# Kernel optimization log

Measured on AMD Instinct MI355X. Metric: run time of the kernel, lower is better.

## Reference

```python
import jax, jax.numpy as jnp
import numpy as np

B, N, GN, GS = 16, 100000, 4096, 64  # batch, points, num_groups, group_size


def setup_inputs() -> dict:
    key = jax.random.key(0)
    k1, k2, k3 = jax.random.split(key, 3)
    x_proto = jax.random.normal(k1, (B, N, 3), dtype=jnp.float32)
    template = jax.random.normal(k2, (N, 3), dtype=jnp.float32)
    groups = jax.random.randint(k3, (GN, GS), 0, N, dtype=jnp.int32)
    return {"x_proto": x_proto, "template": template, "groups": groups}


def reference(x_proto, template, groups):
    # x_proto: [B, N, 3], template: [N, 3], groups: [GN, GS] int indices
    b, n, _ = x_proto.shape
    Yg = template[groups]                      # [GN, GS, 3] gathered template
    Xg = x_proto[:, groups]                    # [B, GN, GS, 3] gathered current points

    # Kabsch: align template group Y to current X (R @ Y + t ~ X)
    muY = Yg.mean(axis=1)                      # [GN, 3]
    muX = Xg.mean(axis=2)                      # [B, GN, 3]
    Yc = Yg - muY[:, None, :]
    Xc = Xg - muX[:, :, None, :]
    H = jnp.einsum('gni,bgnj->bgij', Yc, Xc)   # [B, GN, 3, 3] covariance
    U, S, Vh = jnp.linalg.svd(H)
    V = jnp.swapaxes(Vh, -2, -1)
    R0 = V @ jnp.swapaxes(U, -2, -1)
    det = jnp.linalg.det(R0)                   # [B, GN]
    # flip last column of V where det < 0 to get a proper rotation
    s = jnp.where(det < 0, -1.0, 1.0).astype(x_proto.dtype)
    col_scale = jnp.stack([jnp.ones_like(s), jnp.ones_like(s), s], axis=-1)  # [B, GN, 3]
    R = (V * col_scale[..., None, :]) @ jnp.swapaxes(U, -2, -1)              # [B, GN, 3, 3]
    t = muX - jnp.einsum('bgij,gj->bgi', R, muY)                             # [B, GN, 3]

    # project template group through (R, t)
    Xg_proj = jnp.einsum('bgij,gnj->bgni', R, Yg) + t[:, :, None, :]         # [B, GN, GS, 3]

    # scatter-add with overlap counting, then average
    flat_idx = groups.reshape(-1)              # [GN*GS]
    out = jnp.zeros_like(x_proto).at[:, flat_idx].add(Xg_proj.reshape(b, -1, 3))
    counts = jnp.zeros((n,), dtype=x_proto.dtype).at[flat_idx].add(1.0)
    counts = jnp.maximum(counts, 1.0)
    return out / counts[None, :, None]
```

## Files before the change

### kernel.cpp

```cpp
#include <hip/hip_runtime.h>
#include <math.h>

static constexpr int BB = 16;
static constexpr int NN = 100000;
static constexpr int GN = 4096;
static constexpr int GS = 64;
static constexpr int NP = BB * GN;
static constexpr int SLOT = 32;

__device__ __forceinline__ float wsum64(float v) {
#pragma unroll
  for (int off = 32; off > 0; off >>= 1) v += __shfl_xor(v, off, 64);
  return v;
}

__global__ __launch_bounds__(256) void k_xpad(
    const float4* __restrict__ x, float4* __restrict__ x4,
    int4* __restrict__ cnt4) {
  int t = blockIdx.x * 256 + threadIdx.x;
  if (t < NN / 4) cnt4[t] = make_int4(0, 0, 0, 0);
  if (t >= BB * NN / 4) return;
  float4 a = x[t * 3 + 0], b = x[t * 3 + 1], c = x[t * 3 + 2];
  x4[t * 4 + 0] = make_float4(a.x, a.y, a.z, 0.f);
  x4[t * 4 + 1] = make_float4(a.w, b.x, b.y, 0.f);
  x4[t * 4 + 2] = make_float4(b.z, b.w, c.x, 0.f);
  x4[t * 4 + 3] = make_float4(c.y, c.z, c.w, 0.f);
}

__global__ __launch_bounds__(256) void k_tpl(
    const float* __restrict__ tpl, const int* __restrict__ groups,
    float* __restrict__ Yg, float* __restrict__ GmY,
    int* __restrict__ cnt, int* __restrict__ ent) {
  int g    = blockIdx.x * 4 + (threadIdx.x >> 6);
  int lane = threadIdx.x & 63;
  int idx = groups[g * GS + lane];
  int pos = atomicAdd(&cnt[idx], 1);
  if (pos < SLOT) ent[idx * SLOT + pos] = g;
  float y0 = tpl[idx * 3 + 0], y1 = tpl[idx * 3 + 1], y2 = tpl[idx * 3 + 2];
  float* o = Yg + ((size_t)g * GS + lane) * 3;
  o[0] = y0; o[1] = y1; o[2] = y2;
  float sy0 = wsum64(y0), sy1 = wsum64(y1), sy2 = wsum64(y2);
  if (lane == 0) {
    const float inv = 1.0f / 64.0f;
    *(float4*)(GmY + (size_t)g * 4) =
        make_float4(sy0 * inv, sy1 * inv, sy2 * inv, 0.0f);
  }
}

__global__ __launch_bounds__(256) void k_stats(
    const float4* __restrict__ x4, const float* __restrict__ Yg,
    const float* __restrict__ GmY, const int* __restrict__ groups,
    float* __restrict__ Ht) {
  int bid  = (blockIdx.x & 7) * 512 + (blockIdx.x >> 3);
  int wid4 = bid * 4 + (threadIdx.x >> 6);
  int lane = threadIdx.x & 63;
  int s    = lane >> 4;
  int l4   = lane & 15;
  int p = wid4 * 4 + s;
  int b = p >> 12;
  int g = p & (GN - 1);

  int4 iv = *(const int4*)(groups + (size_t)g * GS + l4 * 4);
  const float4* yv = (const float4*)(Yg + ((size_t)g * GS + l4 * 4) * 3);
  float4 ya = yv[0], yb = yv[1], yc = yv[2];

  const float4* xb4 = x4 + (size_t)b * NN;
  float sx0 = 0.f, sx1 = 0.f, sx2 = 0.f;
  float h00 = 0.f, h01 = 0.f, h02 = 0.f;
  float h10 = 0.f, h11 = 0.f, h12 = 0.f;
  float h20 = 0.f, h21 = 0.f, h22 = 0.f;

#define ACC(Y0, Y1, Y2, IDX)                                   \
  {                                                            \
    float4 xv = xb4[IDX];                                      \
    sx0 += xv.x; sx1 += xv.y; sx2 += xv.z;                     \
    h00 += (Y0) * xv.x; h01 += (Y0) * xv.y; h02 += (Y0) * xv.z;\
    h10 += (Y1) * xv.x; h11 += (Y1) * xv.y; h12 += (Y1) * xv.z;\
    h20 += (Y2) * xv.x; h21 += (Y2) * xv.y; h22 += (Y2) * xv.z;\
  }
  ACC(ya.x, ya.y, ya.z, iv.x);
  ACC(ya.w, yb.x, yb.y, iv.y);
  ACC(yb.z, yb.w, yc.x, iv.z);
  ACC(yc.y, yc.z, yc.w, iv.w);
#undef ACC

#define RED(V)                                                 \
  V += __shfl_xor(V, 8, 64); V += __shfl_xor(V, 4, 64);        \
  V += __shfl_xor(V, 2, 64); V += __shfl_xor(V, 1, 64);
  RED(sx0) RED(sx1) RED(sx2)
  RED(h00) RED(h01) RED(h02)
  RED(h10) RED(h11) RED(h12)
  RED(h20) RED(h21) RED(h22)
#undef RED

  if (l4 == 0) {
    const float inv = 1.0f / 64.0f;
    float4 m = *(const float4*)(GmY + (size_t)g * 4);
    float mx0 = sx0 * inv, mx1 = sx1 * inv, mx2 = sx2 * inv;
    float4 o0 = make_float4(mx0, mx1, mx2, h00 - m.x * sx0);
    float4 o1 = make_float4(h01 - m.x * sx1, h02 - m.x * sx2,
                            h10 - m.y * sx0, h11 - m.y * sx1);
    float4 o2 = make_float4(h12 - m.y * sx2, h20 - m.z * sx0,
                            h21 - m.z * sx1, h22 - m.z * sx2);
    float* o = Ht + (size_t)p * 12;
    *(float4*)(o + 0) = o0;
    *(float4*)(o + 4) = o1;
    *(float4*)(o + 8) = o2;
  }
}

#define JROT(P, Q, RR)                                                        \
  {                                                                           \
    float apq = K[P][Q];                                                      \
    if (fabsf(apq) > 1e-30f) {                                                \
      float app = K[P][P], aqq = K[Q][Q];                                     \
      float tau = (aqq - app) / (2.0f * apq);                                 \
      float tt = copysignf(1.0f, tau) / (fabsf(tau) + sqrtf(1.0f + tau*tau)); \
      float cc = 1.0f / sqrtf(1.0f + tt * tt);                                \
      float ss = tt * cc;                                                     \
      K[P][P] = app - tt * apq;                                               \
      K[Q][Q] = aqq + tt * apq;                                               \
      K[P][Q] = 0.0f; K[Q][P] = 0.0f;                                         \
      float krp = K[RR][P], krq = K[RR][Q];                                   \
      K[RR][P] = cc * krp - ss * krq; K[P][RR] = K[RR][P];                    \
      K[RR][Q] = ss * krp + cc * krq; K[Q][RR] = K[RR][Q];                    \
      float v0p = V[0][P], v0q = V[0][Q];                                     \
      float v1p = V[1][P], v1q = V[1][Q];                                     \
      float v2p = V[2][P], v2q = V[2][Q];                                     \
      V[0][P] = cc * v0p - ss * v0q; V[0][Q] = ss * v0p + cc * v0q;           \
      V[1][P] = cc * v1p - ss * v1q; V[1][Q] = ss * v1p + cc * v1q;           \
      V[2][P] = cc * v2p - ss * v2q; V[2][Q] = ss * v2p + cc * v2q;           \
    }                                                                         \
  }

#define FIN(AA, BBi, CC)                                                      \
  {                                                                           \
    float va0 = V[0][AA], va1 = V[1][AA], va2 = V[2][AA];                     \
    float vb0 = V[0][BBi], vb1 = V[1][BBi], vb2 = V[2][BBi];                  \
    float vc0 = V[0][CC], vc1 = V[1][CC], vc2 = V[2][CC];                     \
    float ua0 = A[0][0]*va0 + A[0][1]*va1 + A[0][2]*va2;                      \
    float ua1 = A[1][0]*va0 + A[1][1]*va1 + A[1][2]*va2;                      \
    float ua2 = A[2][0]*va0 + A[2][1]*va1 + A[2][2]*va2;                      \
    float il = 1.0f / sqrtf(ua0*ua0 + ua1*ua1 + ua2*ua2 + 1e-30f);            \
    ua0 *= il; ua1 *= il; ua2 *= il;                                          \
    float ub0 = A[0][0]*vb0 + A[0][1]*vb1 + A[0][2]*vb2;                      \
    float ub1 = A[1][0]*vb0 + A[1][1]*vb1 + A[1][2]*vb2;                      \
    float ub2 = A[2][0]*vb0 + A[2][1]*vb1 + A[2][2]*vb2;                      \
    il = 1.0f / sqrtf(ub0*ub0 + ub1*ub1 + ub2*ub2 + 1e-30f);                  \
    ub0 *= il; ub1 *= il; ub2 *= il;                                          \
    float dd = ua0*ub0 + ua1*ub1 + ua2*ub2;                                   \
    ub0 -= dd * ua0; ub1 -= dd * ua1; ub2 -= dd * ua2;                        \
    il = 1.0f / sqrtf(ub0*ub0 + ub1*ub1 + ub2*ub2 + 1e-30f);                  \
    ub0 *= il; ub1 *= il; ub2 *= il;                                          \
    float uc0 = ua1*ub2 - ua2*ub1;                                            \
    float uc1 = ua2*ub0 - ua0*ub2;                                            \
    float uc2 = ua0*ub1 - ua1*ub0;                                            \
    R[0][0] = va0*ua0 + vb0*ub0 + dsg*vc0*uc0;                                \
    R[0][1] = va0*ua1 + vb0*ub1 + dsg*vc0*uc1;                                \
    R[0][2] = va0*ua2 + vb0*ub2 + dsg*vc0*uc2;                                \
    R[1][0] = va1*ua0 + vb1*ub0 + dsg*vc1*uc0;                                \
    R[1][1] = va1*ua1 + vb1*ub1 + dsg*vc1*uc1;                                \
    R[1][2] = va1*ua2 + vb1*ub2 + dsg*vc1*uc2;                                \
    R[2][0] = va2*ua0 + vb2*ub0 + dsg*vc2*uc0;                                \
    R[2][1] = va2*ua1 + vb2*ub1 + dsg*vc2*uc1;                                \
    R[2][2] = va2*ua2 + vb2*ub2 + dsg*vc2*uc2;                                \
  }

__global__ __launch_bounds__(256) void k_svd(
    const float* __restrict__ Ht, const float* __restrict__ GmY,
    float* __restrict__ Rt) {
  int p = blockIdx.x * 256 + threadIdx.x;
  if (p >= NP) return;
  int g = p & (GN - 1);
  const float* h = Ht + (size_t)p * 12;
  float4 f0 = *(const float4*)(h + 0);
  float4 f1 = *(const float4*)(h + 4);
  float4 f2 = *(const float4*)(h + 8);
  float4 m  = *(const float4*)(GmY + (size_t)g * 4);
  float mx0 = f0.x, mx1 = f0.y, mx2 = f0.z;
  float my0 = m.x, my1 = m.y, my2 = m.z;
  float A[3][3];
  A[0][0] = f0.w; A[0][1] = f1.x; A[0][2] = f1.y;
  A[1][0] = f1.z; A[1][1] = f1.w; A[1][2] = f2.x;
  A[2][0] = f2.y; A[2][1] = f2.z; A[2][2] = f2.w;

  float K[3][3];
#pragma unroll
  for (int i = 0; i < 3; ++i)
#pragma unroll
    for (int j = 0; j < 3; ++j)
      K[i][j] = A[0][i]*A[0][j] + A[1][i]*A[1][j] + A[2][i]*A[2][j];

  float V[3][3] = {{1.f,0.f,0.f},{0.f,1.f,0.f},{0.f,0.f,1.f}};
#pragma unroll
  for (int sweep = 0; sweep < 5; ++sweep) {
    JROT(0, 1, 2);
    JROT(0, 2, 1);
    JROT(1, 2, 0);
  }

  float d0 = K[0][0], d1 = K[1][1], d2 = K[2][2];
  float detV = V[0][0]*(V[1][1]*V[2][2] - V[1][2]*V[2][1])
             - V[0][1]*(V[1][0]*V[2][2] - V[1][2]*V[2][0])
             + V[0][2]*(V[1][0]*V[2][1] - V[1][1]*V[2][0]);
  float dsg = (detV < 0.0f) ? -1.0f : 1.0f;

  float R[3][3];
  if (d0 <= d1 && d0 <= d2) {
    FIN(1, 2, 0);
  } else if (d1 <= d0 && d1 <= d2) {
    FIN(2, 0, 1);
  } else {
    FIN(0, 1, 2);
  }

  float t0 = mx0 - (R[0][0]*my0 + R[0][1]*my1 + R[0][2]*my2);
  float t1 = mx1 - (R[1][0]*my0 + R[1][1]*my1 + R[1][2]*my2);
  float t2 = mx2 - (R[2][0]*my0 + R[2][1]*my1 + R[2][2]*my2);

  float* o = Rt + (size_t)p * 12;
  o[0] = R[0][0]; o[1] = R[0][1]; o[2] = R[0][2];
  o[3] = R[1][0]; o[4] = R[1][1]; o[5] = R[1][2];
  o[6] = R[2][0]; o[7] = R[2][1]; o[8] = R[2][2];
  o[9] = t0; o[10] = t1; o[11] = t2;
}

__global__ __launch_bounds__(256) void k_gather(
    const float* __restrict__ tpl, const int* __restrict__ cnt,
    const int* __restrict__ ent, const float* __restrict__ Rt,
    float* __restrict__ out) {
  int n  = blockIdx.x * 64 + (threadIdx.x >> 2);
  int j0 = threadIdx.x & 3;
  int b  = blockIdx.y;
  if (n >= NN) return;
  int cn = cnt[n];
  int c  = min(cn, SLOT);
  float y0 = tpl[n * 3 + 0], y1 = tpl[n * 3 + 1], y2 = tpl[n * 3 + 2];
  float p0 = 0.f, p1 = 0.f, p2 = 0.f;
  const float* Rb = Rt + (size_t)b * GN * 12;
  for (int j = j0; j < c; j += 4) {
    int g = ent[n * SLOT + j];
    const float* rt = Rb + (size_t)g * 12;
    float4 r0 = *(const float4*)(rt + 0);
    float4 r1 = *(const float4*)(rt + 4);
    float4 r2 = *(const float4*)(rt + 8);
    p0 += r0.x * y0 + r0.y * y1 + r0.z * y2 + r2.y;
    p1 += r0.w * y0 + r1.x * y1 + r1.y * y2 + r2.z;
    p2 += r1.z * y0 + r1.w * y1 + r2.x * y2 + r2.w;
  }
  p0 += __shfl_xor(p0, 1, 64); p0 += __shfl_xor(p0, 2, 64);
  p1 += __shfl_xor(p1, 1, 64); p1 += __shfl_xor(p1, 2, 64);
  p2 += __shfl_xor(p2, 1, 64); p2 += __shfl_xor(p2, 2, 64);
  if (j0 == 0) {
    float inv = 1.0f / fmaxf((float)cn, 1.0f);
    float* o = out + ((size_t)b * NN + (size_t)n) * 3;
    o[0] = p0 * inv;
    o[1] = p1 * inv;
    o[2] = p2 * inv;
  }
}

extern "C" void kernel_launch(void* const* d_in, const int* in_sizes, int n_in,
                              void* d_out, int out_size, void* d_ws, size_t ws_size,
                              hipStream_t stream) {
  const float* x      = (const float*)d_in[0];
  const float* tpl    = (const float*)d_in[1];
  const int*   groups = (const int*)d_in[2];
  float* out = (float*)d_out;

  char* ws = (char*)d_ws;
  size_t o_x4  = 0;
  size_t o_yg  = 25600000;
  size_t o_ht  = o_yg + 3145728;
  size_t o_gmy = o_ht + 3145728;
  size_t o_cnt = o_gmy + 65536;
  size_t o_ent = o_cnt + 400000;
  float* x4   = (float*)(ws + o_x4);
  float* Yg   = (float*)(ws + o_yg);
  float* Rt   = (float*)(ws + o_yg);
  float* Ht   = (float*)(ws + o_ht);
  float* GmY  = (float*)(ws + o_gmy);
  int*   cnt  = (int*)(ws + o_cnt);
  int*   ent  = (int*)(ws + o_ent);

  k_xpad<<<(BB * NN / 4 + 255) / 256, 256, 0, stream>>>(
      (const float4*)x, (float4*)x4, (int4*)cnt);
  k_tpl<<<GN / 4, 256, 0, stream>>>(tpl, groups, Yg, GmY, cnt, ent);
  k_stats<<<NP / 16, 256, 0, stream>>>((const float4*)x4, Yg, GmY, groups, Ht);
  k_svd<<<NP / 256, 256, 0, stream>>>(Ht, GmY, Rt);
  k_gather<<<dim3((NN + 63) / 64, BB), 256, 0, stream>>>(tpl, cnt, ent, Rt, out);
}
```

Baseline: 118.0 us.

## Replace fixed-slot inverse index with CSR built by scan, fill, and per-point gather

Replaces the fixed 32-slot per-point group list with a compact CSR structure. A wave-level scan with an atomic global offset assigns each point a start, and a separate fill kernel writes group ids. The gather now uses one thread per point instead of four lanes with a shuffle reduction, reads a padded float4 template, and reads a 16-float aligned R|t record stored in its own buffer. This removes the slot cap, which could silently drop overlaps, and shrinks the index memory. The cost is two extra kernel launches, more atomics, and less parallelism per point in the gather.

```diff
diff --git a/kernel.cpp b/kernel.cpp
--- a/kernel.cpp
+++ b/kernel.cpp
@@ -6,7 +6,8 @@
 static constexpr int GN = 4096;
 static constexpr int GS = 64;
 static constexpr int NP = BB * GN;
-static constexpr int SLOT = 32;
+static constexpr int NE = GN * GS;
+static constexpr int NBLK = (NN + 255) / 256;
 
 __device__ __forceinline__ float wsum64(float v) {
 #pragma unroll
@@ -15,10 +16,19 @@
 }
 
 __global__ __launch_bounds__(256) void k_xpad(
-    const float4* __restrict__ x, float4* __restrict__ x4,
-    int4* __restrict__ cnt4) {
+    const float4* __restrict__ x, const float4* __restrict__ tpl,
+    float4* __restrict__ x4, float4* __restrict__ tpl4,
+    int4* __restrict__ cnt4, int* __restrict__ gtotal) {
   int t = blockIdx.x * 256 + threadIdx.x;
-  if (t < NN / 4) cnt4[t] = make_int4(0, 0, 0, 0);
+  if (t == 0) *gtotal = 0;
+  if (t < NN / 4) {
+    cnt4[t] = make_int4(0, 0, 0, 0);
+    float4 a = tpl[t * 3 + 0], b = tpl[t * 3 + 1], c = tpl[t * 3 + 2];
+    tpl4[t * 4 + 0] = make_float4(a.x, a.y, a.z, 0.f);
+    tpl4[t * 4 + 1] = make_float4(a.w, b.x, b.y, 0.f);
+    tpl4[t * 4 + 2] = make_float4(b.z, b.w, c.x, 0.f);
+    tpl4[t * 4 + 3] = make_float4(c.y, c.z, c.w, 0.f);
+  }
   if (t >= BB * NN / 4) return;
   float4 a = x[t * 3 + 0], b = x[t * 3 + 1], c = x[t * 3 + 2];
   x4[t * 4 + 0] = make_float4(a.x, a.y, a.z, 0.f);
@@ -28,18 +38,16 @@
 }
 
 __global__ __launch_bounds__(256) void k_tpl(
-    const float* __restrict__ tpl, const int* __restrict__ groups,
-    float* __restrict__ Yg, float* __restrict__ GmY,
-    int* __restrict__ cnt, int* __restrict__ ent) {
+    const float4* __restrict__ tpl4, const int* __restrict__ groups,
+    float* __restrict__ Yg, float* __restrict__ GmY, int* __restrict__ cnt) {
   int g    = blockIdx.x * 4 + (threadIdx.x >> 6);
   int lane = threadIdx.x & 63;
   int idx = groups[g * GS + lane];
-  int pos = atomicAdd(&cnt[idx], 1);
-  if (pos < SLOT) ent[idx * SLOT + pos] = g;
-  float y0 = tpl[idx * 3 + 0], y1 = tpl[idx * 3 + 1], y2 = tpl[idx * 3 + 2];
+  atomicAdd(&cnt[idx], 1);
+  float4 y = tpl4[idx];
   float* o = Yg + ((size_t)g * GS + lane) * 3;
-  o[0] = y0; o[1] = y1; o[2] = y2;
-  float sy0 = wsum64(y0), sy1 = wsum64(y1), sy2 = wsum64(y2);
+  o[0] = y.x; o[1] = y.y; o[2] = y.z;
+  float sy0 = wsum64(y.x), sy1 = wsum64(y.y), sy2 = wsum64(y.z);
   if (lane == 0) {
     const float inv = 1.0f / 64.0f;
     *(float4*)(GmY + (size_t)g * 4) =
@@ -218,46 +226,71 @@
   float t1 = mx1 - (R[1][0]*my0 + R[1][1]*my1 + R[1][2]*my2);
   float t2 = mx2 - (R[2][0]*my0 + R[2][1]*my1 + R[2][2]*my2);
 
-  float* o = Rt + (size_t)p * 12;
-  o[0] = R[0][0]; o[1] = R[0][1]; o[2] = R[0][2];
-  o[3] = R[1][0]; o[4] = R[1][1]; o[5] = R[1][2];
-  o[6] = R[2][0]; o[7] = R[2][1]; o[8] = R[2][2];
-  o[9] = t0; o[10] = t1; o[11] = t2;
+  float* o = Rt + (size_t)p * 16;
+  *(float4*)(o + 0) = make_float4(R[0][0], R[0][1], R[0][2], R[1][0]);
+  *(float4*)(o + 4) = make_float4(R[1][1], R[1][2], R[2][0], R[2][1]);
+  *(float4*)(o + 8) = make_float4(R[2][2], t0, t1, t2);
+}
+
+__global__ __launch_bounds__(256) void k_alloc(
+    const int* __restrict__ cnt, int* __restrict__ gtotal,
+    int2* __restrict__ rs_cnt, int* __restrict__ cursor) {
+  int t = blockIdx.x * 256 + threadIdx.x;
+  int lane = threadIdx.x & 63;
+  int v = (t < NN) ? cnt[t] : 0;
+  int sc = v;
+#pragma unroll
+  for (int off = 1; off < 64; off <<= 1) {
+    int u = __shfl_up(sc, off, 64);
+    if (lane >= off) sc += u;
+  }
+  int wtotal = __shfl(sc, 63, 64);
+  int base = 0;
+  if (lane == 63) base = atomicAdd(gtotal, wtotal);
+  base = __shfl(base, 63, 64);
+  if (t < NN) {
+    rs_cnt[t] = make_int2(base + sc - v, v);
+    cursor[t] = 0;
+  }
+}
+
+__global__ __launch_bounds__(256) void k_fill(
+    const int* __restrict__ groups, const int2* __restrict__ rs_cnt,
+    int* __restrict__ cursor, int* __restrict__ entries) {
+  int e = blockIdx.x * 256 + threadIdx.x;
+  if (e >= NE) return;
+  int n = groups[e];
+  int pos = atomicAdd(&cursor[n], 1);
+  entries[rs_cnt[n].x + pos] = e >> 6;
 }
 
 __global__ __launch_bounds__(256) void k_gather(
-    const float* __restrict__ tpl, const int* __restrict__ cnt,
-    const int* __restrict__ ent, const float* __restrict__ Rt,
+    const float4* __restrict__ tpl4, const int2* __restrict__ rs_cnt,
+    const int* __restrict__ entries, const float* __restrict__ Rt,
     float* __restrict__ out) {
-  int n  = blockIdx.x * 64 + (threadIdx.x >> 2);
-  int j0 = threadIdx.x & 3;
-  int b  = blockIdx.y;
+  int n = blockIdx.x * 256 + threadIdx.x;
   if (n >= NN) return;
-  int cn = cnt[n];
-  int c  = min(cn, SLOT);
-  float y0 = tpl[n * 3 + 0], y1 = tpl[n * 3 + 1], y2 = tpl[n * 3 + 2];
+  int b = blockIdx.y;
+  int2 rc = rs_cnt[n];
+  int s = rc.x, c = rc.y;
+  float4 y = tpl4[n];
   float p0 = 0.f, p1 = 0.f, p2 = 0.f;
-  const float* Rb = Rt + (size_t)b * GN * 12;
-  for (int j = j0; j < c; j += 4) {
-    int g = ent[n * SLOT + j];
-    const float* rt = Rb + (size_t)g * 12;
+  const float* Rb = Rt + (size_t)b * GN * 16;
+  for (int j = 0; j < c; ++j) {
+    int g = entries[s + j];
+    const float* rt = Rb + (size_t)g * 16;
     float4 r0 = *(const float4*)(rt + 0);
     float4 r1 = *(const float4*)(rt + 4);
     float4 r2 = *(const float4*)(rt + 8);
-    p0 += r0.x * y0 + r0.y * y1 + r0.z * y2 + r2.y;
-    p1 += r0.w * y0 + r1.x * y1 + r1.y * y2 + r2.z;
-    p2 += r1.z * y0 + r1.w * y1 + r2.x * y2 + r2.w;
-  }
-  p0 += __shfl_xor(p0, 1, 64); p0 += __shfl_xor(p0, 2, 64);
-  p1 += __shfl_xor(p1, 1, 64); p1 += __shfl_xor(p1, 2, 64);
-  p2 += __shfl_xor(p2, 1, 64); p2 += __shfl_xor(p2, 2, 64);
-  if (j0 == 0) {
-    float inv = 1.0f / fmaxf((float)cn, 1.0f);
-    float* o = out + ((size_t)b * NN + (size_t)n) * 3;
-    o[0] = p0 * inv;
-    o[1] = p1 * inv;
-    o[2] = p2 * inv;
-  }
+    p0 += r0.x * y.x + r0.y * y.y + r0.z * y.z + r2.y;
+    p1 += r0.w * y.x + r1.x * y.y + r1.y * y.z + r2.z;
+    p2 += r1.z * y.x + r1.w * y.y + r2.x * y.z + r2.w;
+  }
+  float inv = 1.0f / fmaxf((float)c, 1.0f);
+  float* o = out + ((size_t)b * NN + (size_t)n) * 3;
+  o[0] = p0 * inv;
+  o[1] = p1 * inv;
+  o[2] = p2 * inv;
 }
 
 extern "C" void kernel_launch(void* const* d_in, const int* in_sizes, int n_in,
@@ -269,24 +302,37 @@
   float* out = (float*)d_out;
 
   char* ws = (char*)d_ws;
-  size_t o_x4  = 0;
-  size_t o_yg  = 25600000;
-  size_t o_ht  = o_yg + 3145728;
-  size_t o_gmy = o_ht + 3145728;
-  size_t o_cnt = o_gmy + 65536;
-  size_t o_ent = o_cnt + 400000;
-  float* x4   = (float*)(ws + o_x4);
-  float* Yg   = (float*)(ws + o_yg);
-  float* Rt   = (float*)(ws + o_yg);
-  float* Ht   = (float*)(ws + o_ht);
-  float* GmY  = (float*)(ws + o_gmy);
-  int*   cnt  = (int*)(ws + o_cnt);
-  int*   ent  = (int*)(ws + o_ent);
+  size_t o_x4   = 0;
+  size_t o_tpl4 = o_x4 + 25600000;
+  size_t o_yg   = o_tpl4 + 1600000;
+  size_t o_ht   = o_yg + 3145728;
+  size_t o_rt   = o_ht + 3145728;
+  size_t o_gmy  = o_rt + 4194304;
+  size_t o_cnt  = o_gmy + 65536;
+  size_t o_rsc  = o_cnt + 400000;
+  size_t o_cur  = o_rsc + 800000;
+  size_t o_gt   = o_cur + 400000;
+  size_t o_ent  = o_gt + 64;
+  float* x4     = (float*)(ws + o_x4);
+  float* tpl4   = (float*)(ws + o_tpl4);
+  float* Yg     = (float*)(ws + o_yg);
+  float* Ht     = (float*)(ws + o_ht);
+  float* Rt     = (float*)(ws + o_rt);
+  float* GmY    = (float*)(ws + o_gmy);
+  int*   cnt    = (int*)(ws + o_cnt);
+  int2*  rs_cnt = (int2*)(ws + o_rsc);
+  int*   cursor = (int*)(ws + o_cur);
+  int*   gtotal = (int*)(ws + o_gt);
+  int*   entries= (int*)(ws + o_ent);
 
   k_xpad<<<(BB * NN / 4 + 255) / 256, 256, 0, stream>>>(
-      (const float4*)x, (float4*)x4, (int4*)cnt);
-  k_tpl<<<GN / 4, 256, 0, stream>>>(tpl, groups, Yg, GmY, cnt, ent);
+      (const float4*)x, (const float4*)tpl, (float4*)x4, (float4*)tpl4,
+      (int4*)cnt, gtotal);
+  k_tpl<<<GN / 4, 256, 0, stream>>>((const float4*)tpl4, groups, Yg, GmY, cnt);
   k_stats<<<NP / 16, 256, 0, stream>>>((const float4*)x4, Yg, GmY, groups, Ht);
   k_svd<<<NP / 256, 256, 0, stream>>>(Ht, GmY, Rt);
-  k_gather<<<dim3((NN + 63) / 64, BB), 256, 0, stream>>>(tpl, cnt, ent, Rt, out);
-}
+  k_alloc<<<NBLK, 256, 0, stream>>>(cnt, gtotal, rs_cnt, cursor);
+  k_fill<<<NE / 256, 256, 0, stream>>>(groups, rs_cnt, cursor, entries);
+  k_gather<<<dim3(NBLK, BB), 256, 0, stream>>>(
+      (const float4*)tpl4, rs_cnt, entries, Rt, out);
+}
```

Measured after the change: 138.0 us. 16.9% more time.
